# Kernel optimization log

Measured on AMD Instinct MI355X. Metric: run time of the kernel, lower is better.

The kernel has to match this reference:

```python
import jax, jax.numpy as jnp
import numpy as np

VOCAB = 32000
H = 1024
T = 2048


def setup_inputs() -> dict:
    key = jax.random.key(0)
    ks = jax.random.split(key, 6)
    s = 1.0 / np.sqrt(H)  # torch LSTMCell init bound
    return {
        "tokens": jax.random.randint(ks[0], (T,), 0, VOCAB),
        "embedding": jax.random.normal(ks[1], (VOCAB, H), jnp.float32),
        "W_ih": jax.random.uniform(ks[2], (4 * H, H), jnp.float32, -s, s),
        "W_hh": jax.random.uniform(ks[3], (4 * H, H), jnp.float32, -s, s),
        "b_ih": jax.random.uniform(ks[4], (4 * H,), jnp.float32, -s, s),
        "b_hh": jax.random.uniform(ks[5], (4 * H,), jnp.float32, -s, s),
    }


def reference(tokens, embedding, W_ih, W_hh, b_ih, b_hh):
    # Gather all embeddings up front: [T, H]
    xs = embedding[tokens]
    # Precompute input-side gate pre-activations for all timesteps: [T, 4H]
    gx = xs @ W_ih.T + b_ih + b_hh

    def step(carry, gx_t):
        h, c = carry  # each [H]
        gates = gx_t + h @ W_hh.T  # [4H]
        i, f, g, o = jnp.split(gates, 4)
        i = jax.nn.sigmoid(i)
        f = jax.nn.sigmoid(f)
        g = jnp.tanh(g)
        o = jax.nn.sigmoid(o)
        c = f * c + i * g
        h = o * jnp.tanh(c)
        return (h, c), None

    h0 = jnp.zeros((H,), dtype=xs.dtype)
    c0 = jnp.zeros((H,), dtype=xs.dtype)
    (h, c), _ = jax.lax.scan(step, (h0, c0), gx)
    # Original returns LSTMCell hidden tuple with batch dim 1: ([1,H], [1,H])
    return h[None, :], c[None, :]
```

## Files before the change

### kernel.cpp

```cpp
#include <hip/hip_runtime.h>
#include <hip/hip_bf16.h>

#define TT 2048
#define HH 1024
#define GH 4096

__device__ __forceinline__ float sigm(float x){ return 1.0f / (1.0f + __expf(-x)); }

#define BM 128
#define BN 64
#define BK 32

__global__ __launch_bounds__(256) void gemm_simple(
    const int* __restrict__ tokens,
    const float* __restrict__ emb,
    const float* __restrict__ Wih,
    const float* __restrict__ bih,
    const float* __restrict__ bhh,
    float* __restrict__ gx)
{
  __shared__ float As[BM][BK+1];
  __shared__ float Bs[BN][BK+1];
  __shared__ int tok_s[BM];

  const int tid = threadIdx.x;
  const int bn = blockIdx.x;
  const int bm = blockIdx.y;
  const int m0 = bm*BM, n0 = bn*BN;

  if (tid < BM) tok_s[tid] = tokens[m0 + tid];
  __syncthreads();

  const int tm = tid >> 4;
  const int tn = tid & 15;

  float acc[8][4];
  #pragma unroll
  for (int i = 0; i < 8; ++i)
    #pragma unroll
    for (int j = 0; j < 4; ++j) acc[i][j] = 0.0f;

  for (int k0 = 0; k0 < HH; k0 += BK) {
    for (int idx = tid; idx < BM*BK; idx += 256) {
      int r = idx >> 5, c = idx & 31;
      As[r][c] = emb[(size_t)tok_s[r]*HH + k0 + c];
    }
    for (int idx = tid; idx < BN*BK; idx += 256) {
      int r = idx >> 5, c = idx & 31;
      Bs[r][c] = Wih[(size_t)(n0 + r)*HH + k0 + c];
    }
    __syncthreads();
    #pragma unroll
    for (int k = 0; k < BK; ++k) {
      float a[8], b[4];
      #pragma unroll
      for (int i = 0; i < 8; ++i) a[i] = As[tm*8 + i][k];
      #pragma unroll
      for (int j = 0; j < 4; ++j) b[j] = Bs[tn*4 + j][k];
      #pragma unroll
      for (int i = 0; i < 8; ++i)
        #pragma unroll
        for (int j = 0; j < 4; ++j)
          acc[i][j] = fmaf(a[i], b[j], acc[i][j]);
    }
    __syncthreads();
  }

  float bias[4];
  #pragma unroll
  for (int j = 0; j < 4; ++j) {
    int col = n0 + tn*4 + j;
    bias[j] = bih[col] + bhh[col];
  }
  #pragma unroll
  for (int i = 0; i < 8; ++i) {
    int r = m0 + tm*8 + i;
    #pragma unroll
    for (int j = 0; j < 4; ++j)
      gx[(size_t)r*GH + (n0 + tn*4 + j)] = acc[i][j] + bias[j];
  }
}

#define GBLK 64
#define NTH 512
#define HSTRIDE 130

__global__ __launch_bounds__(NTH, 2) void lstm_scan(
    const float* __restrict__ gx,
    const float* __restrict__ Whh,
    unsigned long long* slots,
    float* __restrict__ out)
{
  const int b = blockIdx.x;
  const int tid = threadIdx.x;
  const int s  = tid & 31;
  const int rg = tid >> 5;

  __shared__ float h_lds[32*HSTRIDE];
  __shared__ float gates_lds[64];

  float w[128];
  #pragma unroll
  for (int a = 0; a < 4; ++a) {
    int row = rg*4 + a;
    int jrow = ((row >> 4) << 10) + (b << 4) + (row & 15);
    const float* wr = Whh + (size_t)jrow*HH + s*32;
    #pragma unroll
    for (int q = 0; q < 8; ++q) {
      float4 f4 = ((const float4*)wr)[q];
      w[a*32 + q*4 + 0] = f4.x; w[a*32 + q*4 + 1] = f4.y;
      w[a*32 + q*4 + 2] = f4.z; w[a*32 + q*4 + 3] = f4.w;
    }
  }

  for (int i = tid; i < 32*HSTRIDE; i += NTH) h_lds[i] = 0.0f;
  float c0 = 0.0f, c1 = 0.0f;
  const int i0 = tid, i1 = tid + 512;
  const int p0 = (i0 >> 5)*HSTRIDE + (i0 & 31);
  const int p1 = (i1 >> 5)*HSTRIDE + (i1 & 31);
  const int myrow = rg*4 + s;
  const int myj = ((myrow >> 4) << 10) + (b << 4) + (myrow & 15);
  __syncthreads();

  for (int t = 0; t < TT; ++t) {
    float gxv = 0.0f;
    if (s < 4) gxv = gx[(size_t)t*GH + myj];

    if (t > 0) {
      const unsigned long long* sb = slots + (size_t)(t & 1)*1024;
      const unsigned tg = (unsigned)t;
      unsigned long long v0 = __hip_atomic_load(&sb[i0], __ATOMIC_RELAXED, __HIP_MEMORY_SCOPE_AGENT);
      unsigned long long v1 = __hip_atomic_load(&sb[i1], __ATOMIC_RELAXED, __HIP_MEMORY_SCOPE_AGENT);
      while ((unsigned)(v0 >> 32) != tg)
        v0 = __hip_atomic_load(&sb[i0], __ATOMIC_RELAXED, __HIP_MEMORY_SCOPE_AGENT);
      while ((unsigned)(v1 >> 32) != tg)
        v1 = __hip_atomic_load(&sb[i1], __ATOMIC_RELAXED, __HIP_MEMORY_SCOPE_AGENT);
      h_lds[p0] = __uint_as_float((unsigned)v0);
      h_lds[p1] = __uint_as_float((unsigned)v1);
      __syncthreads();
    }

    float acc0 = 0.f, acc1 = 0.f, acc2 = 0.f, acc3 = 0.f;
    const float* hseg = h_lds + s*HSTRIDE;
    #pragma unroll
    for (int c2 = 0; c2 < 16; ++c2) {
      float2 hv = *(const float2*)(hseg + 2*c2);
      acc0 = fmaf(w[0*32+2*c2], hv.x, acc0); acc0 = fmaf(w[0*32+2*c2+1], hv.y, acc0);
      acc1 = fmaf(w[1*32+2*c2], hv.x, acc1); acc1 = fmaf(w[1*32+2*c2+1], hv.y, acc1);
      acc2 = fmaf(w[2*32+2*c2], hv.x, acc2); acc2 = fmaf(w[2*32+2*c2+1], hv.y, acc2);
      acc3 = fmaf(w[3*32+2*c2], hv.x, acc3); acc3 = fmaf(w[3*32+2*c2+1], hv.y, acc3);
    }
    #pragma unroll
    for (int m = 1; m <= 16; m <<= 1) {
      acc0 += __shfl_xor(acc0, m);
      acc1 += __shfl_xor(acc1, m);
      acc2 += __shfl_xor(acc2, m);
      acc3 += __shfl_xor(acc3, m);
    }
    if (s < 4) {
      float v = acc0;
      if (s == 1) v = acc1; else if (s == 2) v = acc2; else if (s == 3) v = acc3;
      gates_lds[rg*4 + s] = v + gxv;
    }
    __syncthreads();

    if (tid < 8) {
      int n0 = tid*2, n1 = n0 + 1;
      float xi0 = gates_lds[n0],    xi1 = gates_lds[n1];
      float xf0 = gates_lds[16+n0], xf1 = gates_lds[16+n1];
      float xg0 = gates_lds[32+n0], xg1 = gates_lds[32+n1];
      float xo0 = gates_lds[48+n0], xo1 = gates_lds[48+n1];
      c0 = sigm(xf0)*c0 + sigm(xi0)*tanhf(xg0);
      c1 = sigm(xf1)*c1 + sigm(xi1)*tanhf(xg1);
      float h0 = sigm(xo0)*tanhf(c0);
      float h1 = sigm(xo1)*tanhf(c1);
      if (t == TT-1) {
        out[(b<<4)+n0]      = h0;
        out[(b<<4)+n1]      = h1;
        out[1024+(b<<4)+n0] = c0;
        out[1024+(b<<4)+n1] = c1;
      } else {
        unsigned long long* db = slots + (size_t)((t+1)&1)*1024;
        unsigned long long tg = ((unsigned long long)(unsigned)(t+1)) << 32;
        __hip_atomic_store(&db[(b<<4)+n0], tg | (unsigned long long)__float_as_uint(h0),
                           __ATOMIC_RELAXED, __HIP_MEMORY_SCOPE_AGENT);
        __hip_atomic_store(&db[(b<<4)+n1], tg | (unsigned long long)__float_as_uint(h1),
                           __ATOMIC_RELAXED, __HIP_MEMORY_SCOPE_AGENT);
      }
    }
  }
}

__global__ void zero_out(float* out){
  int i = blockIdx.x*256 + threadIdx.x;
  if (i < 2048) out[i] = 0.0f;
}

extern "C" void kernel_launch(void* const* d_in, const int* in_sizes, int n_in,
                              void* d_out, int out_size, void* d_ws, size_t ws_size,
                              hipStream_t stream) {
  (void)in_sizes; (void)n_in; (void)out_size;
  const int* tokens = (const int*)d_in[0];
  const float* emb  = (const float*)d_in[1];
  const float* Wih  = (const float*)d_in[2];
  const float* Whh  = (const float*)d_in[3];
  const float* bih  = (const float*)d_in[4];
  const float* bhh  = (const float*)d_in[5];
  float* out = (float*)d_out;

  unsigned long long* slots = (unsigned long long*)d_ws;
  float* gx = (float*)((char*)d_ws + 16384);
  const size_t needF32 = 16384 + (size_t)TT*GH*sizeof(float);

  hipMemsetAsync(slots, 0, 16384, stream);
  if (ws_size >= needF32) {
    gemm_simple<<<dim3(64,16), dim3(256), 0, stream>>>(tokens, emb, Wih, bih, bhh, gx);
    lstm_scan<<<dim3(GBLK), dim3(NTH), 0, stream>>>(gx, Whh, slots, out);
  } else {
    zero_out<<<dim3(8), dim3(256), 0, stream>>>(out);
  }
}
```

Baseline: 6.655 ms.

## Restructure LSTM scan so each wave owns two hidden units, removing LDS barriers

```diff
diff --git a/kernel.cpp b/kernel.cpp
--- a/kernel.cpp
+++ b/kernel.cpp
@@ -83,7 +83,6 @@
 
 #define GBLK 64
 #define NTH 512
-#define HSTRIDE 130
 
 __global__ __launch_bounds__(NTH, 2) void lstm_scan(
     const float* __restrict__ gx,
@@ -91,101 +90,112 @@
     unsigned long long* slots,
     float* __restrict__ out)
 {
-  const int b = blockIdx.x;
+  const int b   = blockIdx.x;
   const int tid = threadIdx.x;
-  const int s  = tid & 31;
-  const int rg = tid >> 5;
-
-  __shared__ float h_lds[32*HSTRIDE];
-  __shared__ float gates_lds[64];
-
-  float w[128];
-  #pragma unroll
-  for (int a = 0; a < 4; ++a) {
-    int row = rg*4 + a;
-    int jrow = ((row >> 4) << 10) + (b << 4) + (row & 15);
-    const float* wr = Whh + (size_t)jrow*HH + s*32;
-    #pragma unroll
-    for (int q = 0; q < 8; ++q) {
-      float4 f4 = ((const float4*)wr)[q];
-      w[a*32 + q*4 + 0] = f4.x; w[a*32 + q*4 + 1] = f4.y;
-      w[a*32 + q*4 + 2] = f4.z; w[a*32 + q*4 + 3] = f4.w;
-    }
-  }
-
-  for (int i = tid; i < 32*HSTRIDE; i += NTH) h_lds[i] = 0.0f;
-  float c0 = 0.0f, c1 = 0.0f;
-  const int i0 = tid, i1 = tid + 512;
-  const int p0 = (i0 >> 5)*HSTRIDE + (i0 & 31);
-  const int p1 = (i1 >> 5)*HSTRIDE + (i1 & 31);
-  const int myrow = rg*4 + s;
-  const int myj = ((myrow >> 4) << 10) + (b << 4) + (myrow & 15);
-  __syncthreads();
+  const int lane = tid & 63;
+  const int wv   = tid >> 6;
+  const int o0 = (b << 4) + (wv << 1);
+  const int o1 = o0 + 1;
+
+  float w[8][16];
+  #pragma unroll
+  for (int r = 0; r < 8; ++r) {
+    const int jrow = ((r & 3) << 10) + ((r >> 2) ? o1 : o0);
+    const float* wr = Whh + (size_t)jrow * HH + lane;
+    #pragma unroll
+    for (int j = 0; j < 16; ++j)
+      w[r][j] = wr[64 * j];
+  }
+
+  const bool actlane = (lane == 0) || (lane == 32);
+  const int myout = (lane == 0) ? o0 : o1;
+  float cst = 0.0f;
+  float g4[4] = {0.f, 0.f, 0.f, 0.f};
+  if (actlane) {
+    #pragma unroll
+    for (int g = 0; g < 4; ++g) g4[g] = gx[(g << 10) + myout];
+  }
+
+  float h[16];
+  #pragma unroll
+  for (int j = 0; j < 16; ++j) h[j] = 0.0f;
 
   for (int t = 0; t < TT; ++t) {
-    float gxv = 0.0f;
-    if (s < 4) gxv = gx[(size_t)t*GH + myj];
-
     if (t > 0) {
-      const unsigned long long* sb = slots + (size_t)(t & 1)*1024;
+      const unsigned long long* sb = slots + (size_t)(t & 1) * 1024;
       const unsigned tg = (unsigned)t;
-      unsigned long long v0 = __hip_atomic_load(&sb[i0], __ATOMIC_RELAXED, __HIP_MEMORY_SCOPE_AGENT);
-      unsigned long long v1 = __hip_atomic_load(&sb[i1], __ATOMIC_RELAXED, __HIP_MEMORY_SCOPE_AGENT);
-      while ((unsigned)(v0 >> 32) != tg)
-        v0 = __hip_atomic_load(&sb[i0], __ATOMIC_RELAXED, __HIP_MEMORY_SCOPE_AGENT);
-      while ((unsigned)(v1 >> 32) != tg)
-        v1 = __hip_atomic_load(&sb[i1], __ATOMIC_RELAXED, __HIP_MEMORY_SCOPE_AGENT);
-      h_lds[p0] = __uint_as_float((unsigned)v0);
-      h_lds[p1] = __uint_as_float((unsigned)v1);
-      __syncthreads();
-    }
-
-    float acc0 = 0.f, acc1 = 0.f, acc2 = 0.f, acc3 = 0.f;
-    const float* hseg = h_lds + s*HSTRIDE;
-    #pragma unroll
-    for (int c2 = 0; c2 < 16; ++c2) {
-      float2 hv = *(const float2*)(hseg + 2*c2);
-      acc0 = fmaf(w[0*32+2*c2], hv.x, acc0); acc0 = fmaf(w[0*32+2*c2+1], hv.y, acc0);
-      acc1 = fmaf(w[1*32+2*c2], hv.x, acc1); acc1 = fmaf(w[1*32+2*c2+1], hv.y, acc1);
-      acc2 = fmaf(w[2*32+2*c2], hv.x, acc2); acc2 = fmaf(w[2*32+2*c2+1], hv.y, acc2);
-      acc3 = fmaf(w[3*32+2*c2], hv.x, acc3); acc3 = fmaf(w[3*32+2*c2+1], hv.y, acc3);
-    }
-    #pragma unroll
-    for (int m = 1; m <= 16; m <<= 1) {
-      acc0 += __shfl_xor(acc0, m);
-      acc1 += __shfl_xor(acc1, m);
-      acc2 += __shfl_xor(acc2, m);
-      acc3 += __shfl_xor(acc3, m);
-    }
-    if (s < 4) {
-      float v = acc0;
-      if (s == 1) v = acc1; else if (s == 2) v = acc2; else if (s == 3) v = acc3;
-      gates_lds[rg*4 + s] = v + gxv;
-    }
-    __syncthreads();
-
-    if (tid < 8) {
-      int n0 = tid*2, n1 = n0 + 1;
-      float xi0 = gates_lds[n0],    xi1 = gates_lds[n1];
-      float xf0 = gates_lds[16+n0], xf1 = gates_lds[16+n1];
-      float xg0 = gates_lds[32+n0], xg1 = gates_lds[32+n1];
-      float xo0 = gates_lds[48+n0], xo1 = gates_lds[48+n1];
-      c0 = sigm(xf0)*c0 + sigm(xi0)*tanhf(xg0);
-      c1 = sigm(xf1)*c1 + sigm(xi1)*tanhf(xg1);
-      float h0 = sigm(xo0)*tanhf(c0);
-      float h1 = sigm(xo1)*tanhf(c1);
+      unsigned long long v[16];
+      #pragma unroll
+      for (int j = 0; j < 16; ++j)
+        v[j] = __hip_atomic_load(&sb[lane + 64*j], __ATOMIC_RELAXED, __HIP_MEMORY_SCOPE_AGENT);
+      #pragma unroll
+      for (int j = 0; j < 16; ++j)
+        while ((unsigned)(v[j] >> 32) != tg)
+          v[j] = __hip_atomic_load(&sb[lane + 64*j], __ATOMIC_RELAXED, __HIP_MEMORY_SCOPE_AGENT);
+      #pragma unroll
+      for (int j = 0; j < 16; ++j) h[j] = __uint_as_float((unsigned)v[j]);
+    }
+
+    float acc[8];
+    #pragma unroll
+    for (int r = 0; r < 8; ++r) acc[r] = 0.0f;
+    #pragma unroll
+    for (int j = 0; j < 16; ++j) {
+      const float hj = h[j];
+      #pragma unroll
+      for (int r = 0; r < 8; ++r) acc[r] = fmaf(w[r][j], hj, acc[r]);
+    }
+
+    float v4[4];
+    #pragma unroll
+    for (int i = 0; i < 4; ++i) {
+      float lo = acc[2*i], hi = acc[2*i+1];
+      float a = (lane & 1) ? hi : lo;
+      float q = (lane & 1) ? lo : hi;
+      v4[i] = a + __shfl_xor(q, 1);
+    }
+    float v2[2];
+    #pragma unroll
+    for (int i = 0; i < 2; ++i) {
+      float lo = v2[0], hi = v2[0];
+      lo = v4[2*i]; hi = v4[2*i+1];
+      float a = (lane & 2) ? hi : lo;
+      float q = (lane & 2) ? lo : hi;
+      v2[i] = a + __shfl_xor(q, 2);
+    }
+    float v1;
+    {
+      float lo = v2[0], hi = v2[1];
+      float a = (lane & 4) ? hi : lo;
+      float q = (lane & 4) ? lo : hi;
+      v1 = a + __shfl_xor(q, 4);
+    }
+    v1 += __shfl_xor(v1, 8);
+    v1 += __shfl_xor(v1, 16);
+    v1 += __shfl_xor(v1, 32);
+
+    const int base = (lane >= 32) ? 4 : 0;
+    float xi = __shfl(v1, base + 0);
+    float xf = __shfl(v1, base + 1);
+    float xg = __shfl(v1, base + 2);
+    float xo = __shfl(v1, base + 3);
+
+    if (actlane) {
+      xi += g4[0]; xf += g4[1]; xg += g4[2]; xo += g4[3];
+      cst = sigm(xf)*cst + sigm(xi)*tanhf(xg);
+      float hnew = sigm(xo)*tanhf(cst);
       if (t == TT-1) {
-        out[(b<<4)+n0]      = h0;
-        out[(b<<4)+n1]      = h1;
-        out[1024+(b<<4)+n0] = c0;
-        out[1024+(b<<4)+n1] = c1;
+        out[myout]        = hnew;
+        out[1024 + myout] = cst;
       } else {
-        unsigned long long* db = slots + (size_t)((t+1)&1)*1024;
-        unsigned long long tg = ((unsigned long long)(unsigned)(t+1)) << 32;
-        __hip_atomic_store(&db[(b<<4)+n0], tg | (unsigned long long)__float_as_uint(h0),
-                           __ATOMIC_RELAXED, __HIP_MEMORY_SCOPE_AGENT);
-        __hip_atomic_store(&db[(b<<4)+n1], tg | (unsigned long long)__float_as_uint(h1),
-                           __ATOMIC_RELAXED, __HIP_MEMORY_SCOPE_AGENT);
+        unsigned long long* db = slots + (size_t)((t+1) & 1) * 1024;
+        unsigned long long pv =
+            (((unsigned long long)(unsigned)(t+1)) << 32) |
+            (unsigned long long)__float_as_uint(hnew);
+        __hip_atomic_store(&db[myout], pv, __ATOMIC_RELAXED, __HIP_MEMORY_SCOPE_AGENT);
+        #pragma unroll
+        for (int g = 0; g < 4; ++g)
+          g4[g] = gx[(size_t)(t+1)*GH + (g << 10) + myout];
       }
     }
   }
```

Measured after the change: 13.48 ms. +102.6%, slower.

## Store recurrent weights as bf16 in LDS instead of registers

Applied to the files above, without the earlier changes.

```diff
diff --git a/kernel.cpp b/kernel.cpp
--- a/kernel.cpp
+++ b/kernel.cpp
@@ -6,6 +6,12 @@
 #define GH 4096
 
 __device__ __forceinline__ float sigm(float x){ return 1.0f / (1.0f + __expf(-x)); }
+__device__ __forceinline__ float bflo(unsigned v){ return __uint_as_float(v << 16); }
+__device__ __forceinline__ float bfhi(unsigned v){ return __uint_as_float(v & 0xffff0000u); }
+__device__ __forceinline__ unsigned short f2bu(float x){
+  __hip_bfloat16 b = __float2bfloat16(x);
+  return *reinterpret_cast<unsigned short*>(&b);
+}
 
 #define BM 128
 #define BN 64
@@ -52,16 +58,16 @@
     __syncthreads();
     #pragma unroll
     for (int k = 0; k < BK; ++k) {
-      float a[8], b[4];
+      float a[8], bb[4];
       #pragma unroll
       for (int i = 0; i < 8; ++i) a[i] = As[tm*8 + i][k];
       #pragma unroll
-      for (int j = 0; j < 4; ++j) b[j] = Bs[tn*4 + j][k];
+      for (int j = 0; j < 4; ++j) bb[j] = Bs[tn*4 + j][k];
       #pragma unroll
       for (int i = 0; i < 8; ++i)
         #pragma unroll
         for (int j = 0; j < 4; ++j)
-          acc[i][j] = fmaf(a[i], b[j], acc[i][j]);
+          acc[i][j] = fmaf(a[i], bb[j], acc[i][j]);
     }
     __syncthreads();
   }
@@ -84,8 +90,122 @@
 #define GBLK 64
 #define NTH 512
 #define HSTRIDE 130
-
-__global__ __launch_bounds__(NTH, 2) void lstm_scan(
+#define ROWU 257
+
+__global__ __launch_bounds__(NTH) void lstm_scan_lds(
+    const float* __restrict__ gx,
+    const float* __restrict__ Whh,
+    unsigned long long* slots,
+    float* __restrict__ out)
+{
+  extern __shared__ __align__(16) unsigned wdw[];
+  __shared__ float h_lds[32*HSTRIDE];
+  __shared__ float gates_lds[64];
+
+  const int b = blockIdx.x;
+  const int tid = threadIdx.x;
+  const int s  = tid & 31;
+  const int rg = tid >> 5;
+
+  for (int r = 0; r < 64; ++r) {
+    const int jrow = ((r >> 4) << 10) + (b << 4) + (r & 15);
+    const int c0 = tid * 2;
+    const float2 f2 = *(const float2*)(Whh + (size_t)jrow*HH + c0);
+    const unsigned pk = (unsigned)f2bu(f2.x) | ((unsigned)f2bu(f2.y) << 16);
+    const int sT = c0 >> 5, j2 = (c0 & 31) >> 2, d = (c0 >> 1) & 1;
+    wdw[r*(2*ROWU) + (j2*32 + sT)*2 + d] = pk;
+  }
+
+  for (int i = tid; i < 32*HSTRIDE; i += NTH) h_lds[i] = 0.0f;
+  float c0s = 0.0f, c1s = 0.0f;
+  const int i0 = tid, i1 = tid + 512;
+  const int p0 = (i0 >> 5)*HSTRIDE + (i0 & 31);
+  const int p1 = (i1 >> 5)*HSTRIDE + (i1 & 31);
+  const int myrow = rg*4 + s;
+  const int myj = ((myrow >> 4) << 10) + (b << 4) + (myrow & 15);
+  __syncthreads();
+
+  const uint2* wld2 = (const uint2*)wdw;
+
+  for (int t = 0; t < TT; ++t) {
+    float gxv = 0.0f;
+    if (s < 4) gxv = gx[(size_t)t*GH + myj];
+
+    if (t > 0) {
+      const unsigned long long* sb = slots + (size_t)(t & 1)*1024;
+      const unsigned tg = (unsigned)t;
+      unsigned long long v0 = __hip_atomic_load(&sb[i0], __ATOMIC_RELAXED, __HIP_MEMORY_SCOPE_AGENT);
+      unsigned long long v1 = __hip_atomic_load(&sb[i1], __ATOMIC_RELAXED, __HIP_MEMORY_SCOPE_AGENT);
+      while ((unsigned)(v0 >> 32) != tg)
+        v0 = __hip_atomic_load(&sb[i0], __ATOMIC_RELAXED, __HIP_MEMORY_SCOPE_AGENT);
+      while ((unsigned)(v1 >> 32) != tg)
+        v1 = __hip_atomic_load(&sb[i1], __ATOMIC_RELAXED, __HIP_MEMORY_SCOPE_AGENT);
+      h_lds[p0] = __uint_as_float((unsigned)v0);
+      h_lds[p1] = __uint_as_float((unsigned)v1);
+      __syncthreads();
+    }
+
+    float acc0 = 0.f, acc1 = 0.f, acc2 = 0.f, acc3 = 0.f;
+    const float* hseg = h_lds + s*HSTRIDE;
+    #pragma unroll
+    for (int j2 = 0; j2 < 8; ++j2) {
+      const float2 hA = *(const float2*)(hseg + 4*j2);
+      const float2 hB = *(const float2*)(hseg + 4*j2 + 2);
+      const uint2 w0 = wld2[(rg*4 + 0)*ROWU + j2*32 + s];
+      const uint2 w1 = wld2[(rg*4 + 1)*ROWU + j2*32 + s];
+      const uint2 w2 = wld2[(rg*4 + 2)*ROWU + j2*32 + s];
+      const uint2 w3 = wld2[(rg*4 + 3)*ROWU + j2*32 + s];
+      acc0 = fmaf(bflo(w0.x), hA.x, acc0); acc0 = fmaf(bfhi(w0.x), hA.y, acc0);
+      acc0 = fmaf(bflo(w0.y), hB.x, acc0); acc0 = fmaf(bfhi(w0.y), hB.y, acc0);
+      acc1 = fmaf(bflo(w1.x), hA.x, acc1); acc1 = fmaf(bfhi(w1.x), hA.y, acc1);
+      acc1 = fmaf(bflo(w1.y), hB.x, acc1); acc1 = fmaf(bfhi(w1.y), hB.y, acc1);
+      acc2 = fmaf(bflo(w2.x), hA.x, acc2); acc2 = fmaf(bfhi(w2.x), hA.y, acc2);
+      acc2 = fmaf(bflo(w2.y), hB.x, acc2); acc2 = fmaf(bfhi(w2.y), hB.y, acc2);
+      acc3 = fmaf(bflo(w3.x), hA.x, acc3); acc3 = fmaf(bfhi(w3.x), hA.y, acc3);
+      acc3 = fmaf(bflo(w3.y), hB.x, acc3); acc3 = fmaf(bfhi(w3.y), hB.y, acc3);
+    }
+    #pragma unroll
+    for (int m = 1; m <= 16; m <<= 1) {
+      acc0 += __shfl_xor(acc0, m);
+      acc1 += __shfl_xor(acc1, m);
+      acc2 += __shfl_xor(acc2, m);
+      acc3 += __shfl_xor(acc3, m);
+    }
+    if (s < 4) {
+      float v = acc0;
+      if (s == 1) v = acc1; else if (s == 2) v = acc2; else if (s == 3) v = acc3;
+      gates_lds[rg*4 + s] = v + gxv;
+    }
+    __syncthreads();
+
+    if (tid < 8) {
+      int n0 = tid*2, n1 = n0 + 1;
+      float xi0 = gates_lds[n0],    xi1 = gates_lds[n1];
+      float xf0 = gates_lds[16+n0], xf1 = gates_lds[16+n1];
+      float xg0 = gates_lds[32+n0], xg1 = gates_lds[32+n1];
+      float xo0 = gates_lds[48+n0], xo1 = gates_lds[48+n1];
+      c0s = sigm(xf0)*c0s + sigm(xi0)*tanhf(xg0);
+      c1s = sigm(xf1)*c1s + sigm(xi1)*tanhf(xg1);
+      float h0 = sigm(xo0)*tanhf(c0s);
+      float h1 = sigm(xo1)*tanhf(c1s);
+      if (t == TT-1) {
+        out[(b<<4)+n0]      = h0;
+        out[(b<<4)+n1]      = h1;
+        out[1024+(b<<4)+n0] = c0s;
+        out[1024+(b<<4)+n1] = c1s;
+      } else {
+        unsigned long long* db = slots + (size_t)((t+1)&1)*1024;
+        unsigned long long tg = ((unsigned long long)(unsigned)(t+1)) << 32;
+        __hip_atomic_store(&db[(b<<4)+n0], tg | (unsigned long long)__float_as_uint(h0),
+                           __ATOMIC_RELAXED, __HIP_MEMORY_SCOPE_AGENT);
+        __hip_atomic_store(&db[(b<<4)+n1], tg | (unsigned long long)__float_as_uint(h1),
+                           __ATOMIC_RELAXED, __HIP_MEMORY_SCOPE_AGENT);
+      }
+    }
+  }
+}
+
+__global__ __launch_bounds__(NTH, 2) void lstm_scan_reg(
     const float* __restrict__ gx,
     const float* __restrict__ Whh,
     unsigned long long* slots,
@@ -215,7 +335,16 @@
   hipMemsetAsync(slots, 0, 16384, stream);
   if (ws_size >= needF32) {
     gemm_simple<<<dim3(64,16), dim3(256), 0, stream>>>(tokens, emb, Wih, bih, bhh, gx);
-    lstm_scan<<<dim3(GBLK), dim3(NTH), 0, stream>>>(gx, Whh, slots, out);
+    const int dynBytes = 64 * (2*ROWU) * 4;
+    hipError_t e = hipFuncSetAttribute((const void*)lstm_scan_lds,
+                                       hipFuncAttributeMaxDynamicSharedMemorySize,
+                                       dynBytes);
+    if (e == hipSuccess) {
+      lstm_scan_lds<<<dim3(GBLK), dim3(NTH), dynBytes, stream>>>(gx, Whh, slots, out);
+    } else {
+      (void)hipGetLastError();
+      lstm_scan_reg<<<dim3(GBLK), dim3(NTH), 0, stream>>>(gx, Whh, slots, out);
+    }
   } else {
     zero_out<<<dim3(8), dim3(256), 0, stream>>>(out);
   }
```

Result: slower. 7.002 ms (+5.2%).
